# Performance work log

Hardware: AMD Instinct MI355X
Metric: run time of the kernel (lower is better)

Reference implementation:

```python
import jax, jax.numpy as jnp
from jax import lax
import numpy as np

NSTART, NOPEN, NHID, NCLOSE, NLAYERS, KSZ, N = 40, 128, 256, 3, 40, 9, 1024
H_STEP = 0.1
PAD = (KSZ - 1) // 2  # 4 -> same-length conv
EPS = 1e-5


def conv1(x, K):
    # x: (1, Cin, N), K: (Cout, Cin, k); cross-correlation like torch F.conv1d
    return lax.conv_general_dilated(x, K, (1,), [(PAD, PAD)],
                                    dimension_numbers=('NCH', 'OIH', 'NCH'))


def conv1T(x, K):
    # torch F.conv_transpose1d(x, K, padding=PAD) == conv1d with swapped-channel,
    # flipped kernel and padding k-1-PAD (= PAD here since k=9, PAD=4)
    Kt = jnp.flip(jnp.swapaxes(K, 0, 1), -1)
    return lax.conv_general_dilated(x, Kt, (1,), [(PAD, PAD)],
                                    dimension_numbers=('NCH', 'OIH', 'NCH'))


def instance_norm(x):
    # x: (1, C, N); normalize per channel over spatial dim, biased var, no affine
    m = jnp.mean(x, axis=-1, keepdims=True)
    v = jnp.var(x, axis=-1, keepdims=True)
    return (x - m) * lax.rsqrt(v + EPS)


def get_graph_lap(Z):
    # Z: (C, N). Normalized Gaussian-affinity graph Laplacian.
    sq = jnp.sum(Z * Z, axis=0)  # (N,)
    D2 = jnp.maximum(sq[:, None] + sq[None, :] - 2.0 * (Z.T @ Z), 0.0)
    sigma = jnp.mean(D2) + 1e-12
    Wg = jnp.exp(-D2 / sigma)
    deg = jnp.sum(Wg, axis=1)
    Dh = lax.rsqrt(deg)
    L = Dh[:, None] * (jnp.diag(deg) - Wg) * Dh[None, :]
    return L, deg


def double_sym_layer(Z, Wi, Bi, L):
    # Z: (nopen, N), Wi: (2, nhid, nopen, 9), Bi: (2, nopen, 1), L: (N, N)
    A0 = instance_norm(conv1((Z + Bi[0])[None], Wi[0]))
    A1 = instance_norm((conv1((Z + Bi[1])[None], Wi[1])[0] @ L)[None])
    A0 = jax.nn.relu(A0)
    A1 = jax.nn.relu(A1)
    A0 = conv1T(A0, Wi[0])[0]
    A1 = conv1T(A1, Wi[1])[0] @ L.T
    return A0 + A1  # (nopen, N)


def setup_inputs() -> dict:
    key = jax.random.key(0)
    k1, k2, k3, k4, k5 = jax.random.split(key, 5)
    Z = jax.random.normal(k1, (NSTART, N), dtype=jnp.float32)
    stdv_o = 0.001 * NOPEN / NSTART
    Kopen = jax.random.uniform(k2, (NOPEN, NSTART), minval=-stdv_o, maxval=stdv_o, dtype=jnp.float32)
    stdv_c = 0.001 * NCLOSE / NOPEN
    Kclose = jax.random.uniform(k3, (NCLOSE, NOPEN), minval=-stdv_c, maxval=stdv_c, dtype=jnp.float32)
    W = jax.random.uniform(k4, (NLAYERS, 2, NHID, NOPEN, KSZ), minval=-1e-4, maxval=1e-4, dtype=jnp.float32)
    Bias = jax.random.uniform(k5, (NLAYERS, 2, NOPEN, 1), dtype=jnp.float32) * 1e-4
    return {"Z": Z, "Kopen": Kopen, "Kclose": Kclose, "W": W, "Bias": Bias}


def reference(Z, Kopen, Kclose, W, Bias):
    h = H_STEP
    Zc = Kopen @ Z          # (nopen, N)
    Zold = Zc
    L, _ = get_graph_lap(Zc)
    for i in range(NLAYERS):
        if i % 10 == 0:
            L, _ = get_graph_lap(Zc)
        Ai = double_sym_layer(Zc, W[i], Bias[i], L)
        Zc, Zold = 2.0 * Zc - Zold - (h * h) * Ai, Zc  # leapfrog step
    return (Kclose @ Zc, Kclose @ Zold)
```

## Files before the change

### kernel.cpp

```cpp
#include <hip/hip_runtime.h>

#define NN 1024
#define NOPEN 128
#define NHID 256
#define NSTART 40
#define NCLOSE 3
#define NLAYERS 40
#define KSZ 9

static constexpr float H2 = 0.01f;
static constexpr float IN_EPS = 1e-5f;

using floatx4 = __attribute__((ext_vector_type(4))) float;
using bfrag = __attribute__((ext_vector_type(8))) short;

__device__ __forceinline__ ushort f2bf(float f) {
    union { float f; unsigned u; } v; v.f = f;
    unsigned r = v.u + 0x7fffu + ((v.u >> 16) & 1u);
    return (ushort)(r >> 16);
}

__device__ __forceinline__ void prepw_piece(const float* __restrict__ W, ushort* __restrict__ Wf1,
                                            ushort* __restrict__ Wf2, int lb, int lsrc, int tid) {
    if (lb < 72) {
        int z = lb / 36, rem = lb % 36;
        int t = rem >> 2, q = rem & 3;
        const float* Wz = W + (size_t)(lsrc * 2 + z) * (NHID * NOPEN * KSZ);
        ushort* dst = Wf1 + (((size_t)(z * 9 + t) * 64 + q * 16) << 9);
#pragma unroll
        for (int r = 0; r < 32; ++r) {
            int ei = r * 256 + tid;
            int g = q * 4 + (ei >> 11);
            int kc = (ei >> 9) & 3;
            int lm = (ei >> 3) & 15, lq = (ei >> 7) & 3;
            int e = ei & 7;
            int co = g * 16 + lm, ci = kc * 32 + lq * 8 + e;
            dst[ei] = f2bf(Wz[co * (NOPEN * KSZ) + ci * KSZ + t]);
        }
    } else {
        int p2 = lb - 72;
        int z = p2 / 36, rem = p2 % 36;
        int t = rem >> 2, q = rem & 3;
        const float* Wz = W + (size_t)(lsrc * 2 + z) * (NHID * NOPEN * KSZ);
        ushort* dst = Wf2 + (((size_t)(z * 9 + t) * 64 + q * 16) << 9);
#pragma unroll
        for (int r = 0; r < 32; ++r) {
            int ei = r * 256 + tid;
            int fb = q * 16 + (ei >> 9);
            int g = fb >> 3, j = fb & 7;
            int lm = (ei >> 3) & 15, lq = (ei >> 7) & 3;
            int e = ei & 7;
            int ci = g * 16 + lm, co = j * 32 + lq * 8 + e;
            dst[ei] = f2bf(Wz[co * (NOPEN * KSZ) + ci * KSZ + t]);
        }
    }
}

__global__ __launch_bounds__(256) void k_open(const float* __restrict__ Kopen, const float* __restrict__ Z,
                       float* __restrict__ Zc, float* __restrict__ Zold,
                       const float* __restrict__ Bias0, ushort* __restrict__ Zct,
                       ushort* __restrict__ At0, ushort* __restrict__ At1,
                       const float* __restrict__ W, ushort* __restrict__ Wf1,
                       ushort* __restrict__ Wf2, float* __restrict__ sig, float* __restrict__ A1) {
    const int v = blockIdx.x, tid = threadIdx.x;
    if (v < 512) {
        int o = v >> 2, n = (v & 3) * 256 + tid;
        float acc = 0.f;
#pragma unroll
        for (int s = 0; s < NSTART; ++s)
            acc = fmaf(Kopen[o * NSTART + s], Z[s * NN + n], acc);
        Zc[o * NN + n] = acc;
        Zold[o * NN + n] = acc;
#pragma unroll
        for (int z = 0; z < 2; ++z)
            Zct[z * (1032 * 128) + (n + 4) * 128 + o] = f2bf(acc + Bias0[z * NOPEN + o]);
    } else if (v < 656) {
        prepw_piece(W, Wf1, Wf2, v - 512, 0, tid);
    } else if (v == 656) {
        if (tid == 0) sig[0] = 0.f;
        for (int idx = tid; idx < 1024; idx += 256) {
            int z = idx >> 9, rr = idx & 511;
            ushort* Zz = Zct + z * (1032 * 128);
            Zz[rr] = 0; Zz[1028 * 128 + rr] = 0;
        }
        for (int idx = tid; idx < 2048; idx += 256) {
            int a = idx >> 10, rr = idx & 1023;
            ushort* A = a ? At1 : At0;
            A[rr] = 0; A[1028 * 256 + rr] = 0;
        }
    } else {
        int b = v - 657;
        size_t base = (size_t)b * 4096 + tid * 4;
        float4 z4 = {0.f, 0.f, 0.f, 0.f};
#pragma unroll
        for (int r = 0; r < 4; ++r) *(float4*)&A1[base + r * 1024] = z4;
    }
}

__global__ __launch_bounds__(256) void k_d2(const float* __restrict__ Zc,
                                            float* __restrict__ D2, float* __restrict__ sig) {
    __shared__ __align__(16) float Zi[32 * 36];
    __shared__ __align__(16) float Zj[32 * 68];
    __shared__ float sqi[32], sqj[64];
    __shared__ float red[4];
    const int tid = threadIdx.x;
    const int tx = tid & 15, ty = tid >> 4;
    const int j0 = blockIdx.x * 64, i0 = blockIdx.y * 32;
    if (tid < 32) sqi[tid] = 0.f;
    else if (tid < 96) sqj[tid - 32] = 0.f;
    float acc[2][4] = {};
    for (int c0 = 0; c0 < NOPEN; c0 += 32) {
        for (int idx = tid; idx < 32 * 32; idx += 256) {
            int c = idx >> 5, ii = idx & 31;
            Zi[c * 36 + ii] = Zc[(c0 + c) * NN + i0 + ii];
        }
        for (int idx = tid; idx < 32 * 64; idx += 256) {
            int c = idx >> 6, jj = idx & 63;
            Zj[c * 68 + jj] = Zc[(c0 + c) * NN + j0 + jj];
        }
        __syncthreads();
        if (tid < 32) {
            float s = 0.f;
            for (int c = 0; c < 32; ++c) { float x = Zi[c * 36 + tid]; s = fmaf(x, x, s); }
            sqi[tid] += s;
        } else if (tid < 96) {
            int jj = tid - 32;
            float s = 0.f;
            for (int c = 0; c < 32; ++c) { float x = Zj[c * 68 + jj]; s = fmaf(x, x, s); }
            sqj[jj] += s;
        }
#pragma unroll 8
        for (int c = 0; c < 32; ++c) {
            float2 zi = *(const float2*)&Zi[c * 36 + ty * 2];
            float4 zj = *(const float4*)&Zj[c * 68 + tx * 4];
            acc[0][0] = fmaf(zi.x, zj.x, acc[0][0]);
            acc[0][1] = fmaf(zi.x, zj.y, acc[0][1]);
            acc[0][2] = fmaf(zi.x, zj.z, acc[0][2]);
            acc[0][3] = fmaf(zi.x, zj.w, acc[0][3]);
            acc[1][0] = fmaf(zi.y, zj.x, acc[1][0]);
            acc[1][1] = fmaf(zi.y, zj.y, acc[1][1]);
            acc[1][2] = fmaf(zi.y, zj.z, acc[1][2]);
            acc[1][3] = fmaf(zi.y, zj.w, acc[1][3]);
        }
        __syncthreads();
    }
    float part = 0.f;
#pragma unroll
    for (int m = 0; m < 2; ++m) {
        int i = i0 + ty * 2 + m;
        float sqi_v = sqi[ty * 2 + m];
        float4 d;
        d.x = fmaxf(sqi_v + sqj[tx * 4 + 0] - 2.f * acc[m][0], 0.f);
        d.y = fmaxf(sqi_v + sqj[tx * 4 + 1] - 2.f * acc[m][1], 0.f);
        d.z = fmaxf(sqi_v + sqj[tx * 4 + 2] - 2.f * acc[m][2], 0.f);
        d.w = fmaxf(sqi_v + sqj[tx * 4 + 3] - 2.f * acc[m][3], 0.f);
        *(float4*)&D2[(size_t)i * NN + j0 + tx * 4] = d;
        part += (d.x + d.y) + (d.z + d.w);
    }
#pragma unroll
    for (int off = 32; off > 0; off >>= 1) part += __shfl_down(part, off);
    if ((tid & 63) == 0) red[tid >> 6] = part;
    __syncthreads();
    if (tid == 0) atomicAdd(sig, red[0] + red[1] + red[2] + red[3]);
}

__global__ void k_deg(const float* __restrict__ D2, const float* __restrict__ sig,
                      float* __restrict__ Dh) {
    __shared__ float red[4];
    int i = blockIdx.x, tid = threadIdx.x;
    float inv = 1.f / (sig[0] * (1.f / 1048576.f) + 1e-12f);
    float4 v = *(const float4*)&D2[(size_t)i * NN + tid * 4];
    float s = __expf(-v.x * inv) + __expf(-v.y * inv) + __expf(-v.z * inv) + __expf(-v.w * inv);
#pragma unroll
    for (int off = 32; off > 0; off >>= 1) s += __shfl_down(s, off);
    if ((tid & 63) == 0) red[tid >> 6] = s;
    __syncthreads();
    if (tid == 0) Dh[i] = rsqrtf(red[0] + red[1] + red[2] + red[3]);
}

__global__ void k_L(const float* __restrict__ D2, const float* __restrict__ sig,
                    const float* __restrict__ Dh, ushort* __restrict__ Lb) {
    int i = blockIdx.x, tid = threadIdx.x;
    int j = tid * 4;
    float inv = 1.f / (sig[0] * (1.f / 1048576.f) + 1e-12f);
    float dhi = Dh[i];
    float4 v = *(const float4*)&D2[(size_t)i * NN + j];
    float4 dj = *(const float4*)&Dh[j];
    float4 o;
    o.x = -dhi * dj.x * __expf(-v.x * inv);
    o.y = -dhi * dj.y * __expf(-v.y * inv);
    o.z = -dhi * dj.z * __expf(-v.z * inv);
    o.w = -dhi * dj.w * __expf(-v.w * inv);
    if (i == j + 0) o.x += 1.f;
    if (i == j + 1) o.y += 1.f;
    if (i == j + 2) o.z += 1.f;
    if (i == j + 3) o.w += 1.f;
    ushort4 ob; ob.x = f2bf(o.x); ob.y = f2bf(o.y); ob.z = f2bf(o.z); ob.w = f2bf(o.w);
    *(ushort4*)&Lb[(size_t)i * NN + j] = ob;
}

__global__ __launch_bounds__(256) void k_conv(const ushort* __restrict__ Zct,
        const ushort* __restrict__ Wf1, float* __restrict__ C0, ushort* __restrict__ C1b) {
    const int z = blockIdx.z;
    const int p0 = blockIdx.x * 64, co0 = blockIdx.y * 32;
    __shared__ ushort Xs[72 * 136];
    const int tid = threadIdx.x;
    const ushort* Zz = Zct + z * (1032 * 128);
    for (int idx = tid; idx < 1152; idx += 256) {
        int row = idx >> 4, ch = (idx & 15) * 8;
        *(bfrag*)&Xs[row * 136 + ch] = *(const bfrag*)&Zz[(p0 + row) * 128 + ch];
    }
    __syncthreads();
    const int l = tid & 63, wv = tid >> 6;
    const int wm = wv >> 1, wn = wv & 1;
    const int lm = l & 15, lq = l >> 4;
    const ushort* wf = Wf1 + (((size_t)z * 144 + (blockIdx.y * 2 + wm)) << 11) + l * 8;
    floatx4 acc[2] = {};
    bfrag a_cur[4];
#pragma unroll
    for (int kc = 0; kc < 4; ++kc) a_cur[kc] = *(const bfrag*)(wf + (kc << 9));
    for (int t = 0; t < 9; ++t) {
        bfrag a_nxt[4];
        if (t < 8) {
            const ushort* wptr = wf + (size_t)(t + 1) * (16 << 11);
#pragma unroll
            for (int kc = 0; kc < 4; ++kc) a_nxt[kc] = *(const bfrag*)(wptr + (kc << 9));
        }
        const int xbase = (wn * 32 + lm + t) * 136 + lq * 8;
#pragma unroll
        for (int kc = 0; kc < 4; ++kc) {
            bfrag b0 = *(const bfrag*)&Xs[xbase + kc * 32];
            acc[0] = __builtin_amdgcn_mfma_f32_16x16x32_bf16(a_cur[kc], b0, acc[0], 0, 0, 0);
            bfrag b1 = *(const bfrag*)&Xs[xbase + 16 * 136 + kc * 32];
            acc[1] = __builtin_amdgcn_mfma_f32_16x16x32_bf16(a_cur[kc], b1, acc[1], 0, 0, 0);
        }
#pragma unroll
        for (int kc = 0; kc < 4; ++kc) a_cur[kc] = a_nxt[kc];
    }
    const int cog = co0 + wm * 16 + lq * 4;
    const int pg = p0 + wn * 32 + lm;
#pragma unroll
    for (int j = 0; j < 2; ++j)
#pragma unroll
        for (int r = 0; r < 4; ++r) {
            if (z == 0) C0[(cog + r) * NN + pg + j * 16] = acc[j][r];
            else        C1b[(cog + r) * NN + pg + j * 16] = f2bf(acc[j][r]);
        }
}

__global__ __launch_bounds__(256) void k_xl_mfma(const ushort* __restrict__ X,
                                                 const ushort* __restrict__ Lb,
                                                 float* __restrict__ Out) {
    __shared__ __align__(16) ushort As[64 * 136];
    __shared__ __align__(16) ushort Bs[128 * 136];
    const int tid = threadIdx.x;
    const int lane = tid & 63, wave = tid >> 6;
    const int wm = wave >> 1, wn = wave & 1;
    const int n0 = blockIdx.x * 128, m0 = blockIdx.y * 64, kc = blockIdx.z * 128;
    {
        int q = tid;
#pragma unroll
        for (int r = 0; r < 4; ++r, q += 256) {
            int row = q >> 4, ch = (q & 15) * 8;
            *(bfrag*)&As[row * 136 + ch] = *(const bfrag*)&X[(m0 + row) * NN + kc + ch];
        }
        q = tid;
#pragma unroll
        for (int r = 0; r < 8; ++r, q += 256) {
            int row = q >> 4, ch = (q & 15) * 8;
            *(bfrag*)&Bs[row * 136 + ch] = *(const bfrag*)&Lb[(n0 + row) * NN + kc + ch];
        }
    }
    __syncthreads();
    floatx4 acc[2][4] = {};
    const int lrow = (lane & 15) * 136;
    const int koff = (lane >> 4) * 8;
#pragma unroll
    for (int ks = 0; ks < 4; ++ks) {
        bfrag a[2], b[4];
#pragma unroll
        for (int i = 0; i < 2; ++i)
            a[i] = *(const bfrag*)&As[(wm * 32 + i * 16) * 136 + lrow + ks * 32 + koff];
#pragma unroll
        for (int j = 0; j < 4; ++j)
            b[j] = *(const bfrag*)&Bs[(wn * 64 + j * 16) * 136 + lrow + ks * 32 + koff];
#pragma unroll
        for (int i = 0; i < 2; ++i)
#pragma unroll
            for (int j = 0; j < 4; ++j)
                acc[i][j] = __builtin_amdgcn_mfma_f32_16x16x32_bf16(a[i], b[j], acc[i][j], 0, 0, 0);
    }
    const int mg0 = m0 + wm * 32 + (lane >> 4) * 4;
    const int ng0 = n0 + wn * 64 + (lane & 15);
#pragma unroll
    for (int i = 0; i < 2; ++i)
#pragma unroll
        for (int j = 0; j < 4; ++j)
#pragma unroll
            for (int r = 0; r < 4; ++r)
                atomicAdd(&Out[(size_t)(mg0 + i * 16 + r) * NN + ng0 + j * 16], acc[i][j][r]);
}

__global__ void k_inorm(const float* __restrict__ C0, const float* __restrict__ A1,
                        float* __restrict__ Mu, float* __restrict__ Rs) {
    const int c = blockIdx.x, arr = blockIdx.y, tid = threadIdx.x;
    __shared__ float rs[4], rq[4];
    const float* in = arr ? A1 : C0;
    float4 v = *(const float4*)&in[c * NN + tid * 4];
    float s = (v.x + v.y) + (v.z + v.w);
    float q = (v.x * v.x + v.y * v.y) + (v.z * v.z + v.w * v.w);
#pragma unroll
    for (int off = 32; off > 0; off >>= 1) { s += __shfl_down(s, off); q += __shfl_down(q, off); }
    if ((tid & 63) == 0) { rs[tid >> 6] = s; rq[tid >> 6] = q; }
    __syncthreads();
    if (tid == 0) {
        float S = rs[0] + rs[1] + rs[2] + rs[3];
        float Q = rq[0] + rq[1] + rq[2] + rq[3];
        float mean = S * (1.f / NN);
        float var = Q * (1.f / NN) - mean * mean;
        Mu[arr * NHID + c] = mean;
        Rs[arr * NHID + c] = rsqrtf(var + IN_EPS);
    }
}

__global__ __launch_bounds__(256) void k_normT(const float* __restrict__ C0,
        const float* __restrict__ A1, const float* __restrict__ Mu, const float* __restrict__ Rs,
        ushort* __restrict__ At0, ushort* __restrict__ At1) {
    const int arr = blockIdx.z;
    const int p0 = blockIdx.x * 64, co0 = blockIdx.y * 64;
    const float* in = arr ? A1 : C0;
    ushort* out = arr ? At1 : At0;
    __shared__ ushort Ls[64 * 72];
    const int tid = threadIdx.x;
#pragma unroll
    for (int r = 0; r < 4; ++r) {
        int idx = r * 256 + tid;
        int col = idx >> 4, pq = idx & 15;
        int co = co0 + col;
        float4 v = *(const float4*)&in[(size_t)co * NN + p0 + pq * 4];
        float m = Mu[arr * NHID + co], sc = Rs[arr * NHID + co];
        Ls[(pq * 4 + 0) * 72 + col] = f2bf(fmaxf((v.x - m) * sc, 0.f));
        Ls[(pq * 4 + 1) * 72 + col] = f2bf(fmaxf((v.y - m) * sc, 0.f));
        Ls[(pq * 4 + 2) * 72 + col] = f2bf(fmaxf((v.z - m) * sc, 0.f));
        Ls[(pq * 4 + 3) * 72 + col] = f2bf(fmaxf((v.w - m) * sc, 0.f));
    }
    __syncthreads();
#pragma unroll
    for (int r = 0; r < 2; ++r) {
        int idx = r * 256 + tid;
        int row = idx >> 3, ch = (idx & 7) * 8;
        *(bfrag*)&out[(size_t)(p0 + row + 4) * 256 + co0 + ch] = *(const bfrag*)&Ls[row * 72 + ch];
    }
}

__global__ __launch_bounds__(256) void k_convT(const ushort* __restrict__ At0,
        const ushort* __restrict__ At1, const ushort* __restrict__ Wf2,
        float* __restrict__ Tacc, ushort* __restrict__ T1b) {
    const int z = blockIdx.z;
    const int p0 = blockIdx.x * 64, ci0 = blockIdx.y * 16;
    __shared__ ushort Al[72 * 264];
    const ushort* A = z ? At1 : At0;
    const int tid = threadIdx.x;
    for (int idx = tid; idx < 2304; idx += 256) {
        int row = idx >> 5, ch = (idx & 31) * 8;
        *(bfrag*)&Al[row * 264 + ch] = *(const bfrag*)&A[(p0 + row) * 256 + ch];
    }
    __syncthreads();
    const int l = tid & 63, wv = tid >> 6;
    const int lm = l & 15, lq = l >> 4;
    const ushort* wf = Wf2 + (((size_t)z * 72 + blockIdx.y) << 12) + l * 8;
    floatx4 acc0 = {}, acc1 = {};
    bfrag a_cur[8];
#pragma unroll
    for (int j = 0; j < 8; ++j) a_cur[j] = *(const bfrag*)(wf + (j << 9));
    for (int t = 0; t < 9; ++t) {
        bfrag a_nxt[8];
        if (t < 8) {
            const ushort* wptr = wf + (size_t)(t + 1) * (8 << 12);
#pragma unroll
            for (int j = 0; j < 8; ++j) a_nxt[j] = *(const bfrag*)(wptr + (j << 9));
        }
        const int abase = (wv * 16 + lm + 8 - t) * 264 + lq * 8;
#pragma unroll
        for (int j = 0; j < 8; j += 2) {
            bfrag b0 = *(const bfrag*)&Al[abase + j * 32];
            acc0 = __builtin_amdgcn_mfma_f32_16x16x32_bf16(a_cur[j], b0, acc0, 0, 0, 0);
            bfrag b1 = *(const bfrag*)&Al[abase + j * 32 + 32];
            acc1 = __builtin_amdgcn_mfma_f32_16x16x32_bf16(a_cur[j + 1], b1, acc1, 0, 0, 0);
        }
#pragma unroll
        for (int j = 0; j < 8; ++j) a_cur[j] = a_nxt[j];
    }
    floatx4 acc = acc0 + acc1;
    const int cig = ci0 + lq * 4;
    const int pg = p0 + wv * 16 + lm;
#pragma unroll
    for (int r = 0; r < 4; ++r) {
        if (z == 0) Tacc[(cig + r) * NN + pg] = acc[r];
        else        T1b[(cig + r) * NN + pg] = f2bf(acc[r]);
    }
}

__global__ __launch_bounds__(256) void k_leap(const float* __restrict__ Tacc,
        const float* __restrict__ Zc, float* __restrict__ Zo,
        const float* __restrict__ BiasN, ushort* __restrict__ Zct,
        const float* __restrict__ W, ushort* __restrict__ Wf1, ushort* __restrict__ Wf2,
        float* __restrict__ A1, float* __restrict__ sig, int lnext, int doprep) {
    const int v = blockIdx.x, tid = threadIdx.x;
    if (v < 128) {
        int off = (v * 256 + tid) * 4;
        float4 a = *(const float4*)&Tacc[off];
        float4 zc = *(const float4*)&Zc[off];
        float4 zo = *(const float4*)&Zo[off];
        float4 zn;
        zn.x = 2.f * zc.x - zo.x - H2 * a.x;
        zn.y = 2.f * zc.y - zo.y - H2 * a.y;
        zn.z = 2.f * zc.z - zo.z - H2 * a.z;
        zn.w = 2.f * zc.w - zo.w - H2 * a.w;
        *(float4*)&Zo[off] = zn;
        int ci = off >> 10, n = off & 1023;
#pragma unroll
        for (int z = 0; z < 2; ++z) {
            float bz = BiasN[z * NOPEN + ci];
            ushort* Zz = Zct + z * (1032 * 128);
            Zz[(n + 4) * 128 + ci] = f2bf(zn.x + bz);
            Zz[(n + 5) * 128 + ci] = f2bf(zn.y + bz);
            Zz[(n + 6) * 128 + ci] = f2bf(zn.z + bz);
            Zz[(n + 7) * 128 + ci] = f2bf(zn.w + bz);
        }
    } else if (v < 272) {
        if (doprep) prepw_piece(W, Wf1, Wf2, v - 128, lnext, tid);
    } else if (v == 272) {
        if (tid == 0) sig[0] = 0.f;
    } else {
        int b = v - 273;
        size_t base = (size_t)b * 4096 + tid * 4;
        float4 z4 = {0.f, 0.f, 0.f, 0.f};
#pragma unroll
        for (int r = 0; r < 4; ++r) *(float4*)&A1[base + r * 1024] = z4;
    }
}

__global__ void k_close(const float* __restrict__ Kclose, const float* __restrict__ Zc,
                        const float* __restrict__ Zold, float* __restrict__ out) {
    int n = blockIdx.x * 256 + threadIdx.x;
    int o = blockIdx.y;
    const float* Zb = blockIdx.z ? Zold : Zc;
    float a = 0.f;
#pragma unroll
    for (int c = 0; c < NOPEN; ++c) a = fmaf(Kclose[o * NOPEN + c], Zb[c * NN + n], a);
    out[blockIdx.z * (NCLOSE * NN) + o * NN + n] = a;
}

extern "C" void kernel_launch(void* const* d_in, const int* in_sizes, int n_in,
                              void* d_out, int out_size, void* d_ws, size_t ws_size,
                              hipStream_t stream) {
    const float* Z      = (const float*)d_in[0];
    const float* Kopen  = (const float*)d_in[1];
    const float* Kclose = (const float*)d_in[2];
    const float* W      = (const float*)d_in[3];
    const float* Bias   = (const float*)d_in[4];
    float* out = (float*)d_out;
    float* ws  = (float*)d_ws;

    float* Zb0   = ws + 0;
    float* Zb1   = ws + 131072;
    float* D2    = ws + 262144;
    float* C0    = ws + 1310720;
    float* A1    = ws + 1572864;
    float* Tacc  = ws + 1835008;
    float* Dh    = ws + 5111808;
    float* sig   = ws + 5112832;
    float* Mu    = ws + 5113856;
    float* Rs    = ws + 5114880;
    ushort* Lb  = (ushort*)(ws + 5115904);
    ushort* C1b = (ushort*)(ws + 5640192);
    ushort* T1b = (ushort*)(ws + 5771264);
    ushort* Zct = (ushort*)(ws + 5836800);
    ushort* At0 = (ushort*)(ws + 5968896);
    ushort* At1 = (ushort*)(ws + 6100992);
    ushort* Wf1 = (ushort*)(ws + 6233088);
    ushort* Wf2 = (ushort*)(ws + 6528000);

    k_open<<<dim3(721), 256, 0, stream>>>(Kopen, Z, Zb0, Zb1, Bias, Zct, At0, At1,
                                          W, Wf1, Wf2, sig, A1);

    float* Zc = Zb0;
    float* Zold = Zb1;
    for (int i = 0; i < NLAYERS; ++i) {
        if (i % 10 == 0) {
            k_d2<<<dim3(16, 32), 256, 0, stream>>>(Zc, D2, sig);
            k_deg<<<dim3(NN), 256, 0, stream>>>(D2, sig, Dh);
            k_L<<<dim3(NN), 256, 0, stream>>>(D2, sig, Dh, Lb);
        }
        k_conv<<<dim3(16, 8, 2), 256, 0, stream>>>(Zct, Wf1, C0, C1b);
        k_xl_mfma<<<dim3(8, 4, 8), 256, 0, stream>>>(C1b, Lb, A1);
        k_inorm<<<dim3(NHID, 2), 256, 0, stream>>>(C0, A1, Mu, Rs);
        k_normT<<<dim3(16, 4, 2), 256, 0, stream>>>(C0, A1, Mu, Rs, At0, At1);
        k_convT<<<dim3(16, 8, 2), 256, 0, stream>>>(At0, At1, Wf2, Tacc, T1b);
        k_xl_mfma<<<dim3(8, 2, 8), 256, 0, stream>>>(T1b, Lb, Tacc);
        int lnext = (i + 1 < NLAYERS) ? i + 1 : NLAYERS - 1;
        k_leap<<<dim3(337), 256, 0, stream>>>(Tacc, Zc, Zold,
                                              Bias + (size_t)lnext * 2 * NOPEN, Zct,
                                              W, Wf1, Wf2, A1, sig, lnext, (i + 1 < NLAYERS) ? 1 : 0);
        float* tmp = Zc; Zc = Zold; Zold = tmp;
    }

    k_close<<<dim3(4, NCLOSE, 2), 256, 0, stream>>>(Kclose, Zc, Zold, out);
}
```

Baseline: 2.092 ms.

## Halve tile sizes across conv, matmul and norm kernels and split-K convT

Halves the spatial tile in k_conv, k_normT and k_convT and the N tile in k_xl_mfma, doubling the grid sizes so more blocks run in parallel on the many CUs. k_convT also splits its 256-wide channel reduction across two wave pairs and adds the partial sums through shared memory before writing. The aim is better occupancy and load balance for these small per-layer kernels. The cost is more redundant halo and weight loads per output, extra synchronization, and more atomics in the matmul.

```diff
diff --git a/kernel.cpp b/kernel.cpp
--- a/kernel.cpp
+++ b/kernel.cpp
@@ -202,11 +202,11 @@
 __global__ __launch_bounds__(256) void k_conv(const ushort* __restrict__ Zct,
         const ushort* __restrict__ Wf1, float* __restrict__ C0, ushort* __restrict__ C1b) {
     const int z = blockIdx.z;
-    const int p0 = blockIdx.x * 64, co0 = blockIdx.y * 32;
-    __shared__ ushort Xs[72 * 136];
+    const int p0 = blockIdx.x * 32, co0 = blockIdx.y * 32;
+    __shared__ ushort Xs[40 * 136];
     const int tid = threadIdx.x;
     const ushort* Zz = Zct + z * (1032 * 128);
-    for (int idx = tid; idx < 1152; idx += 256) {
+    for (int idx = tid; idx < 640; idx += 256) {
         int row = idx >> 4, ch = (idx & 15) * 8;
         *(bfrag*)&Xs[row * 136 + ch] = *(const bfrag*)&Zz[(p0 + row) * 128 + ch];
     }
@@ -215,7 +215,7 @@
     const int wm = wv >> 1, wn = wv & 1;
     const int lm = l & 15, lq = l >> 4;
     const ushort* wf = Wf1 + (((size_t)z * 144 + (blockIdx.y * 2 + wm)) << 11) + l * 8;
-    floatx4 acc[2] = {};
+    floatx4 acc = {};
     bfrag a_cur[4];
 #pragma unroll
     for (int kc = 0; kc < 4; ++kc) a_cur[kc] = *(const bfrag*)(wf + (kc << 9));
@@ -226,37 +226,33 @@
 #pragma unroll
             for (int kc = 0; kc < 4; ++kc) a_nxt[kc] = *(const bfrag*)(wptr + (kc << 9));
         }
-        const int xbase = (wn * 32 + lm + t) * 136 + lq * 8;
+        const int xbase = (wn * 16 + lm + t) * 136 + lq * 8;
 #pragma unroll
         for (int kc = 0; kc < 4; ++kc) {
             bfrag b0 = *(const bfrag*)&Xs[xbase + kc * 32];
-            acc[0] = __builtin_amdgcn_mfma_f32_16x16x32_bf16(a_cur[kc], b0, acc[0], 0, 0, 0);
-            bfrag b1 = *(const bfrag*)&Xs[xbase + 16 * 136 + kc * 32];
-            acc[1] = __builtin_amdgcn_mfma_f32_16x16x32_bf16(a_cur[kc], b1, acc[1], 0, 0, 0);
+            acc = __builtin_amdgcn_mfma_f32_16x16x32_bf16(a_cur[kc], b0, acc, 0, 0, 0);
         }
 #pragma unroll
         for (int kc = 0; kc < 4; ++kc) a_cur[kc] = a_nxt[kc];
     }
     const int cog = co0 + wm * 16 + lq * 4;
-    const int pg = p0 + wn * 32 + lm;
-#pragma unroll
-    for (int j = 0; j < 2; ++j)
-#pragma unroll
-        for (int r = 0; r < 4; ++r) {
-            if (z == 0) C0[(cog + r) * NN + pg + j * 16] = acc[j][r];
-            else        C1b[(cog + r) * NN + pg + j * 16] = f2bf(acc[j][r]);
-        }
+    const int pg = p0 + wn * 16 + lm;
+#pragma unroll
+    for (int r = 0; r < 4; ++r) {
+        if (z == 0) C0[(cog + r) * NN + pg] = acc[r];
+        else        C1b[(cog + r) * NN + pg] = f2bf(acc[r]);
+    }
 }
 
 __global__ __launch_bounds__(256) void k_xl_mfma(const ushort* __restrict__ X,
                                                  const ushort* __restrict__ Lb,
                                                  float* __restrict__ Out) {
     __shared__ __align__(16) ushort As[64 * 136];
-    __shared__ __align__(16) ushort Bs[128 * 136];
+    __shared__ __align__(16) ushort Bs[64 * 136];
     const int tid = threadIdx.x;
     const int lane = tid & 63, wave = tid >> 6;
     const int wm = wave >> 1, wn = wave & 1;
-    const int n0 = blockIdx.x * 128, m0 = blockIdx.y * 64, kc = blockIdx.z * 128;
+    const int n0 = blockIdx.x * 64, m0 = blockIdx.y * 64, kc = blockIdx.z * 128;
     {
         int q = tid;
 #pragma unroll
@@ -266,36 +262,36 @@
         }
         q = tid;
 #pragma unroll
-        for (int r = 0; r < 8; ++r, q += 256) {
+        for (int r = 0; r < 4; ++r, q += 256) {
             int row = q >> 4, ch = (q & 15) * 8;
             *(bfrag*)&Bs[row * 136 + ch] = *(const bfrag*)&Lb[(n0 + row) * NN + kc + ch];
         }
     }
     __syncthreads();
-    floatx4 acc[2][4] = {};
+    floatx4 acc[2][2] = {};
     const int lrow = (lane & 15) * 136;
     const int koff = (lane >> 4) * 8;
 #pragma unroll
     for (int ks = 0; ks < 4; ++ks) {
-        bfrag a[2], b[4];
+        bfrag a[2], b[2];
 #pragma unroll
         for (int i = 0; i < 2; ++i)
             a[i] = *(const bfrag*)&As[(wm * 32 + i * 16) * 136 + lrow + ks * 32 + koff];
 #pragma unroll
-        for (int j = 0; j < 4; ++j)
-            b[j] = *(const bfrag*)&Bs[(wn * 64 + j * 16) * 136 + lrow + ks * 32 + koff];
+        for (int j = 0; j < 2; ++j)
+            b[j] = *(const bfrag*)&Bs[(wn * 32 + j * 16) * 136 + lrow + ks * 32 + koff];
 #pragma unroll
         for (int i = 0; i < 2; ++i)
 #pragma unroll
-            for (int j = 0; j < 4; ++j)
+            for (int j = 0; j < 2; ++j)
                 acc[i][j] = __builtin_amdgcn_mfma_f32_16x16x32_bf16(a[i], b[j], acc[i][j], 0, 0, 0);
     }
     const int mg0 = m0 + wm * 32 + (lane >> 4) * 4;
-    const int ng0 = n0 + wn * 64 + (lane & 15);
+    const int ng0 = n0 + wn * 32 + (lane & 15);
 #pragma unroll
     for (int i = 0; i < 2; ++i)
 #pragma unroll
-        for (int j = 0; j < 4; ++j)
+        for (int j = 0; j < 2; ++j)
 #pragma unroll
             for (int r = 0; r < 4; ++r)
                 atomicAdd(&Out[(size_t)(mg0 + i * 16 + r) * NN + ng0 + j * 16], acc[i][j][r]);
@@ -327,15 +323,15 @@
         const float* __restrict__ A1, const float* __restrict__ Mu, const float* __restrict__ Rs,
         ushort* __restrict__ At0, ushort* __restrict__ At1) {
     const int arr = blockIdx.z;
-    const int p0 = blockIdx.x * 64, co0 = blockIdx.y * 64;
+    const int p0 = blockIdx.x * 32, co0 = blockIdx.y * 64;
     const float* in = arr ? A1 : C0;
     ushort* out = arr ? At1 : At0;
-    __shared__ ushort Ls[64 * 72];
+    __shared__ ushort Ls[32 * 72];
     const int tid = threadIdx.x;
 #pragma unroll
-    for (int r = 0; r < 4; ++r) {
+    for (int r = 0; r < 2; ++r) {
         int idx = r * 256 + tid;
-        int col = idx >> 4, pq = idx & 15;
+        int col = idx >> 3, pq = idx & 7;
         int co = co0 + col;
         float4 v = *(const float4*)&in[(size_t)co * NN + p0 + pq * 4];
         float m = Mu[arr * NHID + co], sc = Rs[arr * NHID + co];
@@ -345,10 +341,8 @@
         Ls[(pq * 4 + 3) * 72 + col] = f2bf(fmaxf((v.w - m) * sc, 0.f));
     }
     __syncthreads();
-#pragma unroll
-    for (int r = 0; r < 2; ++r) {
-        int idx = r * 256 + tid;
-        int row = idx >> 3, ch = (idx & 7) * 8;
+    {
+        int row = tid >> 3, ch = (tid & 7) * 8;
         *(bfrag*)&out[(size_t)(p0 + row + 4) * 256 + co0 + ch] = *(const bfrag*)&Ls[row * 72 + ch];
     }
 }
@@ -357,47 +351,59 @@
         const ushort* __restrict__ At1, const ushort* __restrict__ Wf2,
         float* __restrict__ Tacc, ushort* __restrict__ T1b) {
     const int z = blockIdx.z;
-    const int p0 = blockIdx.x * 64, ci0 = blockIdx.y * 16;
-    __shared__ ushort Al[72 * 264];
+    const int p0 = blockIdx.x * 32, ci0 = blockIdx.y * 16;
+    __shared__ ushort Al[40 * 264];
+    __shared__ float Red[2][64][4];
     const ushort* A = z ? At1 : At0;
     const int tid = threadIdx.x;
-    for (int idx = tid; idx < 2304; idx += 256) {
+    for (int idx = tid; idx < 1280; idx += 256) {
         int row = idx >> 5, ch = (idx & 31) * 8;
         *(bfrag*)&Al[row * 264 + ch] = *(const bfrag*)&A[(p0 + row) * 256 + ch];
     }
     __syncthreads();
     const int l = tid & 63, wv = tid >> 6;
+    const int ph = wv & 1, kh = wv >> 1;
     const int lm = l & 15, lq = l >> 4;
-    const ushort* wf = Wf2 + (((size_t)z * 72 + blockIdx.y) << 12) + l * 8;
+    const ushort* wbase = Wf2 + (((size_t)z * 72 + blockIdx.y) << 12) + ((kh * 4) << 9) + l * 8;
     floatx4 acc0 = {}, acc1 = {};
-    bfrag a_cur[8];
-#pragma unroll
-    for (int j = 0; j < 8; ++j) a_cur[j] = *(const bfrag*)(wf + (j << 9));
+    bfrag a_cur[4];
+#pragma unroll
+    for (int jj = 0; jj < 4; ++jj) a_cur[jj] = *(const bfrag*)(wbase + (jj << 9));
     for (int t = 0; t < 9; ++t) {
-        bfrag a_nxt[8];
+        bfrag a_nxt[4];
         if (t < 8) {
-            const ushort* wptr = wf + (size_t)(t + 1) * (8 << 12);
-#pragma unroll
-            for (int j = 0; j < 8; ++j) a_nxt[j] = *(const bfrag*)(wptr + (j << 9));
-        }
-        const int abase = (wv * 16 + lm + 8 - t) * 264 + lq * 8;
-#pragma unroll
-        for (int j = 0; j < 8; j += 2) {
-            bfrag b0 = *(const bfrag*)&Al[abase + j * 32];
-            acc0 = __builtin_amdgcn_mfma_f32_16x16x32_bf16(a_cur[j], b0, acc0, 0, 0, 0);
-            bfrag b1 = *(const bfrag*)&Al[abase + j * 32 + 32];
-            acc1 = __builtin_amdgcn_mfma_f32_16x16x32_bf16(a_cur[j + 1], b1, acc1, 0, 0, 0);
-        }
-#pragma unroll
-        for (int j = 0; j < 8; ++j) a_cur[j] = a_nxt[j];
+            const ushort* wptr = wbase + (size_t)(t + 1) * (8 << 12);
+#pragma unroll
+            for (int jj = 0; jj < 4; ++jj) a_nxt[jj] = *(const bfrag*)(wptr + (jj << 9));
+        }
+        const int abase = (ph * 16 + lm + 8 - t) * 264 + lq * 8;
+#pragma unroll
+        for (int jj = 0; jj < 4; jj += 2) {
+            bfrag b0 = *(const bfrag*)&Al[abase + (kh * 4 + jj) * 32];
+            acc0 = __builtin_amdgcn_mfma_f32_16x16x32_bf16(a_cur[jj], b0, acc0, 0, 0, 0);
+            bfrag b1 = *(const bfrag*)&Al[abase + (kh * 4 + jj + 1) * 32];
+            acc1 = __builtin_amdgcn_mfma_f32_16x16x32_bf16(a_cur[jj + 1], b1, acc1, 0, 0, 0);
+        }
+#pragma unroll
+        for (int jj = 0; jj < 4; ++jj) a_cur[jj] = a_nxt[jj];
     }
     floatx4 acc = acc0 + acc1;
-    const int cig = ci0 + lq * 4;
-    const int pg = p0 + wv * 16 + lm;
-#pragma unroll
-    for (int r = 0; r < 4; ++r) {
-        if (z == 0) Tacc[(cig + r) * NN + pg] = acc[r];
-        else        T1b[(cig + r) * NN + pg] = f2bf(acc[r]);
+    __syncthreads();
+    if (kh == 1) {
+#pragma unroll
+        for (int r = 0; r < 4; ++r) Red[ph][l][r] = acc[r];
+    }
+    __syncthreads();
+    if (kh == 0) {
+#pragma unroll
+        for (int r = 0; r < 4; ++r) acc[r] += Red[ph][l][r];
+        const int cig = ci0 + lq * 4;
+        const int pg = p0 + ph * 16 + lm;
+#pragma unroll
+        for (int r = 0; r < 4; ++r) {
+            if (z == 0) Tacc[(cig + r) * NN + pg] = acc[r];
+            else        T1b[(cig + r) * NN + pg] = f2bf(acc[r]);
+        }
     }
 }
 
@@ -493,16 +499,17 @@
             k_deg<<<dim3(NN), 256, 0, stream>>>(D2, sig, Dh);
             k_L<<<dim3(NN), 256, 0, stream>>>(D2, sig, Dh, Lb);
         }
-        k_conv<<<dim3(16, 8, 2), 256, 0, stream>>>(Zct, Wf1, C0, C1b);
-        k_xl_mfma<<<dim3(8, 4, 8), 256, 0, stream>>>(C1b, Lb, A1);
+        k_conv<<<dim3(32, 8, 2), 256, 0, stream>>>(Zct, Wf1, C0, C1b);
+        k_xl_mfma<<<dim3(16, 4, 8), 256, 0, stream>>>(C1b, Lb, A1);
         k_inorm<<<dim3(NHID, 2), 256, 0, stream>>>(C0, A1, Mu, Rs);
-        k_normT<<<dim3(16, 4, 2), 256, 0, stream>>>(C0, A1, Mu, Rs, At0, At1);
-        k_convT<<<dim3(16, 8, 2), 256, 0, stream>>>(At0, At1, Wf2, Tacc, T1b);
-        k_xl_mfma<<<dim3(8, 2, 8), 256, 0, stream>>>(T1b, Lb, Tacc);
+        k_normT<<<dim3(32, 4, 2), 256, 0, stream>>>(C0, A1, Mu, Rs, At0, At1);
+        k_convT<<<dim3(32, 8, 2), 256, 0, stream>>>(At0, At1, Wf2, Tacc, T1b);
+        k_xl_mfma<<<dim3(16, 2, 8), 256, 0, stream>>>(T1b, Lb, Tacc);
         int lnext = (i + 1 < NLAYERS) ? i + 1 : NLAYERS - 1;
         k_leap<<<dim3(337), 256, 0, stream>>>(Tacc, Zc, Zold,
                                               Bias + (size_t)lnext * 2 * NOPEN, Zct,
-                                              W, Wf1, Wf2, A1, sig, lnext, (i + 1 < NLAYERS) ? 1 : 0);
+                                              W, Wf1, Wf2, A1, sig, lnext,
+                                              (i + 1 < NLAYERS) ? 1 : 0);
         float* tmp = Zc; Zc = Zold; Zold = tmp;
     }
 
```

After: 1.874 ms. 1.12x faster.
